# Kernel tuning notes

Measured on AMD Instinct MI355X. Metric: run time of the kernel, lower is better.

Reference implementation:

```python
import jax, jax.numpy as jnp
import numpy as np

NUM_EMBEDDINGS = 1024
EMBEDDING_DIM = 64
COMMITMENT_COST = 0.25


def setup_inputs() -> dict:
    key = jax.random.key(0)
    k1, k2 = jax.random.split(key)
    z = jax.random.normal(k1, (32, EMBEDDING_DIM, 32, 32), dtype=jnp.float32)
    # matches nn.Embedding init: uniform(-1/K, 1/K)
    codebook = jax.random.uniform(
        k2, (NUM_EMBEDDINGS, EMBEDDING_DIM), dtype=jnp.float32,
        minval=-1.0 / NUM_EMBEDDINGS, maxval=1.0 / NUM_EMBEDDINGS)
    return {"z": z, "codebook": codebook}


def reference(z, codebook):
    B, C, H, W = z.shape  # C == embedding_dim
    zp = jnp.transpose(z, (0, 2, 3, 1))          # [B,H,W,C]
    z_flat = zp.reshape(-1, C)                    # [N,C], N=B*H*W
    # squared euclidean distances to every code: [N,K]
    d = (jnp.sum(z_flat ** 2, axis=1, keepdims=True)
         + jnp.sum(codebook ** 2, axis=1)
         - 2.0 * jnp.matmul(z_flat, codebook.T))
    indices = jnp.argmin(d, axis=1)               # [N]
    z_q = codebook[indices].reshape(zp.shape)     # [B,H,W,C]
    e_latent_loss = jnp.mean((jax.lax.stop_gradient(z_q) - zp) ** 2)
    q_latent_loss = jnp.mean((z_q - jax.lax.stop_gradient(zp)) ** 2)
    loss = q_latent_loss + COMMITMENT_COST * e_latent_loss
    # straight-through estimator
    z_q_st = zp + jax.lax.stop_gradient(z_q - zp)
    z_q_out = jnp.transpose(z_q_st, (0, 3, 1, 2))  # back to NCHW
    return z_q_out, loss, indices
```

## Files before the change

### kernel.cpp

```cpp
#include <hip/hip_runtime.h>
#include <float.h>


#define DIM       64
#define N_EMB     1024
#define LOSS_OFF  2097152
#define IDX_OFF   2097153
#define LOSS_SCALE 5.9604644775390625e-07f

__device__ __forceinline__ float np_sumsq64(const float* a) {
    #pragma clang fp contract(off)
    float r[8];
    #pragma unroll
    for (int j = 0; j < 8; ++j) {
        float s = a[j] * a[j];
        #pragma unroll
        for (int m = 1; m < 8; ++m) {
            float p = a[j + 8 * m] * a[j + 8 * m];
            s = s + p;
        }
        r[j] = s;
    }
    return ((r[0] + r[1]) + (r[2] + r[3])) + ((r[4] + r[5]) + (r[6] + r[7]));
}

__global__ __launch_bounds__(512, 4)
void vq_main(const float* __restrict__ z, const float* __restrict__ cb,
             float* __restrict__ out, float* __restrict__ ws_partial) {
    __shared__ float esq[N_EMB];
    __shared__ float cand_val[8 * 64];
    __shared__ int   cand_idx[8 * 64];
    __shared__ int   fidx[64];
    __shared__ float lred[8];

    const int tid  = threadIdx.x;
    const int lane = tid & 63;
    const int wave = __builtin_amdgcn_readfirstlane(tid >> 6);
    const int n0   = blockIdx.x * 64;
    const int b    = n0 >> 10;
    const int hw0  = n0 & 1023;
    const size_t zbase = (size_t)b * 65536 + (size_t)hw0;

    {
        #pragma clang fp contract(off)
        for (int t = 0; t < 2; ++t) {
            const int k = tid * 2 + t;
            float a[DIM];
            const float4* row = (const float4*)(cb + (size_t)k * DIM);
            #pragma unroll
            for (int j = 0; j < 16; ++j) ((float4*)a)[j] = row[j];
            esq[k] = np_sumsq64(a);
        }
    }

    float vz[DIM];
    #pragma unroll
    for (int c = 0; c < DIM; ++c)
        vz[c] = z[zbase + (size_t)c * 1024 + lane];
    const float zz = np_sumsq64(vz);

    __syncthreads();

    float best = FLT_MAX;
    int   bidx = 0;
    const int kbase = wave * 128;
    for (int k = kbase; k < kbase + 128; k += 2) {
        const float* e0 = cb + (size_t)k * DIM;
        const float* e1 = e0 + DIM;
        float d0 = 0.f, d1 = 0.f;
        #pragma unroll
        for (int c = 0; c < DIM; ++c) {
            d0 = __builtin_fmaf(e0[c], vz[c], d0);
            d1 = __builtin_fmaf(e1[c], vz[c], d1);
        }
        float s0, s1;
        {
            #pragma clang fp contract(off)
            const float p0 = zz + esq[k];
            const float p1 = zz + esq[k + 1];
            s0 = p0 - 2.0f * d0;
            s1 = p1 - 2.0f * d1;
        }
        if (s0 < best) { best = s0; bidx = k; }
        if (s1 < best) { best = s1; bidx = k + 1; }
    }
    cand_val[wave * 64 + lane] = best;
    cand_idx[wave * 64 + lane] = bidx;
    __syncthreads();

    if (tid < 64) {
        float bv = cand_val[tid];
        int   bi = cand_idx[tid];
        #pragma unroll
        for (int w = 1; w < 8; ++w) {
            float v = cand_val[w * 64 + tid];
            int   i = cand_idx[w * 64 + tid];
            if (v < bv || (v == bv && i < bi)) { bv = v; bi = i; }
        }
        fidx[tid] = bi;
        out[IDX_OFF + n0 + tid] = (float)bi;
    }
    __syncthreads();

    const int px = tid & 63;
    const int cg = tid >> 6;
    const int mi = fidx[px];
    float lacc = 0.f;
    #pragma unroll
    for (int i = 0; i < 8; ++i) {
        const int c = cg * 8 + i;
        float q  = cb[mi * DIM + c];
        size_t go = zbase + (size_t)c * 1024 + px;
        float zv = z[go];
        float d  = q - zv;
        lacc = __builtin_fmaf(d, d, lacc);
        out[go] = q;
    }
    #pragma unroll
    for (int off = 32; off > 0; off >>= 1)
        lacc += __shfl_down(lacc, off, 64);
    if (lane == 0) lred[wave] = lacc;
    __syncthreads();
    if (tid == 0) {
        float t = 0.f;
        #pragma unroll
        for (int w = 0; w < 8; ++w) t += lred[w];
        ws_partial[blockIdx.x] = t;
    }
}

__global__ __launch_bounds__(512)
void vq_loss_finalize(const float* __restrict__ ws_partial, float* __restrict__ out) {
    __shared__ float red[8];
    const int tid = threadIdx.x;
    float v = ws_partial[tid];
    #pragma unroll
    for (int off = 32; off > 0; off >>= 1)
        v += __shfl_down(v, off, 64);
    const int lane = tid & 63, wave = tid >> 6;
    if (lane == 0) red[wave] = v;
    __syncthreads();
    if (tid == 0) {
        float t = 0.f;
        #pragma unroll
        for (int w = 0; w < 8; ++w) t += red[w];
        out[LOSS_OFF] = t * LOSS_SCALE;
    }
}

extern "C" void kernel_launch(void* const* d_in, const int* in_sizes, int n_in,
                              void* d_out, int out_size, void* d_ws, size_t ws_size,
                              hipStream_t stream) {
    const float* z  = (const float*)d_in[0];
    const float* cb = (const float*)d_in[1];
    float* out = (float*)d_out;
    float* ws  = (float*)d_ws;

    vq_main<<<512, 512, 0, stream>>>(z, cb, out, ws);
    vq_loss_finalize<<<1, 512, 0, stream>>>(ws, out);
}
```

Baseline: 156.6 us.

## Stage z tile in swizzled LDS and block distance loop over 8 codes

Wave 0 alone now loads the 64-pixel z tile, computes each pixel's squared norm, and writes the tile into XOR-swizzled shared memory. Previously every wave reloaded all 64 channels from global memory into registers. The distance loop processes 8 codebook rows per iteration and reads z vectors as float4 from LDS, which cuts register pressure and raises reuse of each loaded z value. The loss epilogue reads z from LDS instead of global memory. In exchange, LDS use grows by 16 KB, which may limit occupancy, and the distance loop adds LDS reads.

```diff
diff --git a/kernel.cpp b/kernel.cpp
--- a/kernel.cpp
+++ b/kernel.cpp
@@ -8,30 +8,17 @@
 #define IDX_OFF   2097153
 #define LOSS_SCALE 5.9604644775390625e-07f
 
-__device__ __forceinline__ float np_sumsq64(const float* a) {
-    #pragma clang fp contract(off)
-    float r[8];
-    #pragma unroll
-    for (int j = 0; j < 8; ++j) {
-        float s = a[j] * a[j];
-        #pragma unroll
-        for (int m = 1; m < 8; ++m) {
-            float p = a[j + 8 * m] * a[j + 8 * m];
-            s = s + p;
-        }
-        r[j] = s;
-    }
-    return ((r[0] + r[1]) + (r[2] + r[3])) + ((r[4] + r[5]) + (r[6] + r[7]));
-}
-
 __global__ __launch_bounds__(512, 4)
 void vq_main(const float* __restrict__ z, const float* __restrict__ cb,
              float* __restrict__ out, float* __restrict__ ws_partial) {
-    __shared__ float esq[N_EMB];
-    __shared__ float cand_val[8 * 64];
-    __shared__ int   cand_idx[8 * 64];
-    __shared__ int   fidx[64];
-    __shared__ float lred[8];
+    __shared__ float  esq[N_EMB];
+    __shared__ float4 vzl4[64 * 16];
+    __shared__ float  zzs[64];
+    __shared__ float  cand_val[8 * 64];
+    __shared__ int    cand_idx[8 * 64];
+    __shared__ int    fidx[64];
+    __shared__ float  lred[8];
+    float* vzl = (float*)vzl4;
 
     const int tid  = threadIdx.x;
     const int lane = tid & 63;
@@ -45,44 +32,79 @@
         #pragma clang fp contract(off)
         for (int t = 0; t < 2; ++t) {
             const int k = tid * 2 + t;
-            float a[DIM];
             const float4* row = (const float4*)(cb + (size_t)k * DIM);
+            float r[8];
             #pragma unroll
-            for (int j = 0; j < 16; ++j) ((float4*)a)[j] = row[j];
-            esq[k] = np_sumsq64(a);
+            for (int m = 0; m < 8; ++m) {
+                const float4 x0 = row[2 * m];
+                const float4 x1 = row[2 * m + 1];
+                const float a[8] = {x0.x, x0.y, x0.z, x0.w,
+                                    x1.x, x1.y, x1.z, x1.w};
+                #pragma unroll
+                for (int j = 0; j < 8; ++j) {
+                    const float p = a[j] * a[j];
+                    if (m == 0) r[j] = p; else r[j] = r[j] + p;
+                }
+            }
+            esq[k] = ((r[0] + r[1]) + (r[2] + r[3]))
+                   + ((r[4] + r[5]) + (r[6] + r[7]));
         }
     }
 
-    float vz[DIM];
-    #pragma unroll
-    for (int c = 0; c < DIM; ++c)
-        vz[c] = z[zbase + (size_t)c * 1024 + lane];
-    const float zz = np_sumsq64(vz);
-
+    if (wave == 0) {
+        #pragma clang fp contract(off)
+        const int sw = (lane & 7) << 2;
+        float r[8];
+        #pragma unroll
+        for (int m = 0; m < 8; ++m) {
+            float a[8];
+            #pragma unroll
+            for (int j = 0; j < 8; ++j)
+                a[j] = z[zbase + (size_t)(8 * m + j) * 1024 + lane];
+            #pragma unroll
+            for (int j = 0; j < 8; ++j) {
+                const float p = a[j] * a[j];
+                if (m == 0) r[j] = p; else r[j] = r[j] + p;
+            }
+            const int w0 = lane * DIM + ((8 * m)     ^ sw);
+            const int w1 = lane * DIM + ((8 * m + 4) ^ sw);
+            *(float4*)&vzl[w0] = make_float4(a[0], a[1], a[2], a[3]);
+            *(float4*)&vzl[w1] = make_float4(a[4], a[5], a[6], a[7]);
+        }
+        zzs[lane] = ((r[0] + r[1]) + (r[2] + r[3]))
+                  + ((r[4] + r[5]) + (r[6] + r[7]));
+    }
     __syncthreads();
 
+    const float zz = zzs[lane];
+    const int   sw = (lane & 7) << 2;
     float best = FLT_MAX;
     int   bidx = 0;
     const int kbase = wave * 128;
-    for (int k = kbase; k < kbase + 128; k += 2) {
-        const float* e0 = cb + (size_t)k * DIM;
-        const float* e1 = e0 + DIM;
-        float d0 = 0.f, d1 = 0.f;
+    for (int k = kbase; k < kbase + 128; k += 8) {
+        const float* e = cb + (size_t)k * DIM;
+        float d[8] = {0.f, 0.f, 0.f, 0.f, 0.f, 0.f, 0.f, 0.f};
         #pragma unroll
-        for (int c = 0; c < DIM; ++c) {
-            d0 = __builtin_fmaf(e0[c], vz[c], d0);
-            d1 = __builtin_fmaf(e1[c], vz[c], d1);
+        for (int t = 0; t < 16; ++t) {
+            const float4 v = *(const float4*)&vzl[lane * DIM + ((4 * t) ^ sw)];
+            const float va[4] = {v.x, v.y, v.z, v.w};
+            #pragma unroll
+            for (int j = 0; j < 4; ++j) {
+                const int c = 4 * t + j;
+                #pragma unroll
+                for (int q = 0; q < 8; ++q)
+                    d[q] = __builtin_fmaf(e[q * DIM + c], va[j], d[q]);
+            }
         }
-        float s0, s1;
         {
             #pragma clang fp contract(off)
-            const float p0 = zz + esq[k];
-            const float p1 = zz + esq[k + 1];
-            s0 = p0 - 2.0f * d0;
-            s1 = p1 - 2.0f * d1;
+            #pragma unroll
+            for (int q = 0; q < 8; ++q) {
+                const float p = zz + esq[k + q];
+                const float s = p - 2.0f * d[q];
+                if (s < best) { best = s; bidx = k + q; }
+            }
         }
-        if (s0 < best) { best = s0; bidx = k; }
-        if (s1 < best) { best = s1; bidx = k + 1; }
     }
     cand_val[wave * 64 + lane] = best;
     cand_idx[wave * 64 + lane] = bidx;
@@ -110,10 +132,10 @@
     for (int i = 0; i < 8; ++i) {
         const int c = cg * 8 + i;
         float q  = cb[mi * DIM + c];
+        float zv = vzl[px * DIM + (c ^ ((px & 7) << 2))];
         size_t go = zbase + (size_t)c * 1024 + px;
-        float zv = z[go];
-        float d  = q - zv;
-        lacc = __builtin_fmaf(d, d, lacc);
+        float dd = q - zv;
+        lacc = __builtin_fmaf(dd, dd, lacc);
         out[go] = q;
     }
     #pragma unroll
```

Result: slower. 522.8 us (+233.8%).
